# Kernel optimization log

Hardware: AMD Instinct MI355X
Metric: run time of the kernel (lower is better)

The kernel has to match this reference:

```python
import jax, jax.numpy as jnp
import numpy as np

NDIM = 1024
NHEAD = 16
HEAD_DIM = NDIM // NHEAD


def setup_inputs() -> dict:
    key = jax.random.key(0)
    ks = jax.random.split(key, 12)
    B, L, C = 2, 2048, NDIM
    s = 0.02
    return {
        "q": jax.random.normal(ks[0], (B, L, C), jnp.float32),
        "k": jax.random.normal(ks[1], (B, L, C), jnp.float32),
        "v": jax.random.normal(ks[2], (B, L, C), jnp.float32),
        "Wq": jax.random.normal(ks[3], (C, C), jnp.float32) * s,
        "bq": jax.random.normal(ks[4], (C,), jnp.float32) * s,
        "Wk": jax.random.normal(ks[5], (C, C), jnp.float32) * s,
        "bk": jax.random.normal(ks[6], (C,), jnp.float32) * s,
        "Wv": jax.random.normal(ks[7], (C, C), jnp.float32) * s,
        "bv": jax.random.normal(ks[8], (C,), jnp.float32) * s,
        "Wo": jax.random.normal(ks[9], (C, C), jnp.float32) * s,
        "bo": jax.random.normal(ks[10], (C,), jnp.float32) * s,
    }


def reference(q, k, v, Wq, bq, Wk, bk, Wv, bv, Wo, bo):
    B, Lq, C = q.shape
    H, D = NHEAD, HEAD_DIM
    # projections, then split heads: (B, H, L, D)
    qh = (q @ Wq + bq).reshape(B, Lq, H, D).transpose(0, 2, 1, 3)
    kh = (k @ Wk + bk).reshape(B, k.shape[1], H, D).transpose(0, 2, 1, 3)
    vh = (v @ Wv + bv).reshape(B, v.shape[1], H, D).transpose(0, 2, 1, 3)
    scale = 1.0 / jnp.sqrt(jnp.asarray(D, qh.dtype))
    att = jnp.einsum("bhqd,bhkd->bhqk", qh, kh) * scale  # (B,H,Lq,Lk)
    att = jax.nn.softmax(att, axis=-1)  # dropout p=0.0 -> identity
    y = jnp.einsum("bhqk,bhkd->bhqd", att, vh)
    y = y.transpose(0, 2, 1, 3).reshape(B, Lq, C)
    return y @ Wo + bo
```

## Files before the change

### kernel.cpp

```cpp
#include <hip/hip_runtime.h>
#include <math.h>

#define BATCH 2
#define SEQ   2048
#define CDIM  1024
#define NHEAD 16
#define HDIM  64
#define TOKS  (BATCH * SEQ)

typedef __bf16 bf16x8 __attribute__((ext_vector_type(8)));
typedef __bf16 bf16x2 __attribute__((ext_vector_type(2)));
typedef float  f32x4  __attribute__((ext_vector_type(4)));
typedef float  f32x16 __attribute__((ext_vector_type(16)));

#define MFMA16(a, b, c) __builtin_amdgcn_mfma_f32_16x16x32_bf16(a, b, c, 0, 0, 0)
#define MFMA32(a, b, c) __builtin_amdgcn_mfma_f32_32x32x16_bf16(a, b, c, 0, 0, 0)

#define QSCALE 0.1803368801111204f

__device__ __forceinline__ void gload_lds16(const __bf16* g, __bf16* l) {
    __builtin_amdgcn_global_load_lds(
        (const __attribute__((address_space(1))) unsigned int*)g,
        (__attribute__((address_space(3))) unsigned int*)l, 16, 0, 0);
}

__global__ __launch_bounds__(256) void prep_kernel(
    const float* __restrict__ q, const float* __restrict__ k, const float* __restrict__ v,
    __bf16* __restrict__ qo, __bf16* __restrict__ ko, __bf16* __restrict__ vo,
    const float* __restrict__ W0, const float* __restrict__ W1,
    const float* __restrict__ W2, const float* __restrict__ W3,
    __bf16* __restrict__ T0, __bf16* __restrict__ T1,
    __bf16* __restrict__ T2, __bf16* __restrict__ T3)
{
    __shared__ __bf16 Ts[64][72];
    const int bx = blockIdx.x;
    const int tid = threadIdx.x;

    if (bx < 6144) {
        const int t = bx >> 11;
        const size_t i = ((size_t)(bx & 2047) * 256 + tid) * 8;
        const float* s = t == 0 ? q : (t == 1 ? k : v);
        __bf16* d = t == 0 ? qo : (t == 1 ? ko : vo);
        const float4 x = *(const float4*)&s[i];
        const float4 y = *(const float4*)&s[i + 4];
        bf16x8 o;
        o[0] = (__bf16)x.x; o[1] = (__bf16)x.y; o[2] = (__bf16)x.z; o[3] = (__bf16)x.w;
        o[4] = (__bf16)y.x; o[5] = (__bf16)y.y; o[6] = (__bf16)y.z; o[7] = (__bf16)y.w;
        *(bf16x8*)&d[i] = o;
        return;
    }

    const int t  = bx - 6144;
    const int z  = t >> 8;
    const int ry = (t & 255) >> 4;
    const int rx = t & 15;
    const float* W = z == 0 ? W0 : z == 1 ? W1 : z == 2 ? W2 : W3;
    __bf16* T = z == 0 ? T0 : z == 1 ? T1 : z == 2 ? T2 : T3;
    const int rb = ry * 64, cb = rx * 64;
    const int r = tid >> 4;
    const int c4 = (tid & 15) * 4;
#pragma unroll
    for (int p = 0; p < 4; p++) {
        const int rr = p * 16 + r;
        const float4 w4 = *(const float4*)&W[(size_t)(rb + rr) * CDIM + cb + c4];
        Ts[c4 + 0][rr] = (__bf16)w4.x;
        Ts[c4 + 1][rr] = (__bf16)w4.y;
        Ts[c4 + 2][rr] = (__bf16)w4.z;
        Ts[c4 + 3][rr] = (__bf16)w4.w;
    }
    __syncthreads();
    const int n = tid >> 2;
    const int k16 = (tid & 3) * 16;
    *(bf16x8*)&T[(size_t)(cb + n) * CDIM + rb + k16]     = *(const bf16x8*)&Ts[n][k16];
    *(bf16x8*)&T[(size_t)(cb + n) * CDIM + rb + k16 + 8] = *(const bf16x8*)&Ts[n][k16 + 8];
}

__global__ __launch_bounds__(512, 6) void qkv_gemm_kernel(
    const __bf16* __restrict__ qb, const __bf16* __restrict__ kb,
    const __bf16* __restrict__ vb,
    const __bf16* __restrict__ Wqt, const __bf16* __restrict__ Wkt,
    const __bf16* __restrict__ Wvt,
    const float* __restrict__ bq, const float* __restrict__ bk,
    const float* __restrict__ bv,
    __bf16* __restrict__ Qh, __bf16* __restrict__ Kh, __bf16* __restrict__ Vht)
{
    __shared__ __bf16 As[128 * 32];
    __shared__ __bf16 Bs[128 * 32];

    const int lin = blockIdx.x + (blockIdx.y << 3) + (blockIdx.z << 8);
    const int nl  = (lin & 7) * 96 + (lin >> 3);
    const int bx  = nl & 7;
    const int by  = (nl >> 3) & 31;
    const int z   = nl >> 8;

    const __bf16* A    = z == 0 ? qb : z == 1 ? kb : Wvt;
    const __bf16* Bt   = z == 0 ? Wqt : z == 1 ? Wkt : vb;
    const float*  bias = z == 0 ? bq : z == 1 ? bk : bv;

    const int tid  = threadIdx.x;
    const int w    = tid >> 6;
    const int lane = tid & 63;
    const int quad = lane >> 4;
    const int c    = lane & 15;
    const int wm   = w >> 1;
    const int wn   = w & 1;
    const int rowBase = (z == 2 ? bx : by) * 128;
    const int colBase = (z == 2 ? by : bx) * 128;

    const int sr = lane >> 2;
    const int sk = (lane & 3) * 8;

    f32x4 acc[2][4];
#pragma unroll
    for (int i = 0; i < 2; i++)
#pragma unroll
        for (int j = 0; j < 4; j++) acc[i][j] = (f32x4){0, 0, 0, 0};

    const __bf16* srcA = A  + (size_t)(rowBase + w * 16 + sr) * CDIM + sk;
    const __bf16* srcB = Bt + (size_t)(colBase + w * 16 + sr) * CDIM + sk;
    __bf16* dstA = &As[w * 16 * 32];
    __bf16* dstB = &Bs[w * 16 * 32];

    for (int k0 = 0; k0 < CDIM; k0 += 32) {
        gload_lds16(srcA + k0, dstA);
        gload_lds16(srcB + k0, dstB);
        __syncthreads();

        bf16x8 af[2], bf[4];
#pragma unroll
        for (int i = 0; i < 2; i++)
            af[i] = *(const bf16x8*)&As[(wm * 32 + i * 16 + c) * 32 + quad * 8];
#pragma unroll
        for (int i = 0; i < 4; i++)
            bf[i] = *(const bf16x8*)&Bs[(wn * 64 + i * 16 + c) * 32 + quad * 8];
#pragma unroll
        for (int mi = 0; mi < 2; mi++)
#pragma unroll
            for (int ni = 0; ni < 4; ni++)
                acc[mi][ni] = MFMA16(af[mi], bf[ni], acc[mi][ni]);
        __syncthreads();
    }

#pragma unroll
    for (int mi = 0; mi < 2; mi++) {
#pragma unroll
        for (int ni = 0; ni < 4; ni++) {
            const int col = colBase + wn * 64 + ni * 16 + c;
#pragma unroll
            for (int r = 0; r < 4; r++) {
                const int row = rowBase + wm * 32 + mi * 16 + quad * 4 + r;
                const float val = acc[mi][ni][r];
                if (z == 2) {
                    Vht[(size_t)row * TOKS + col] = (__bf16)(val + bias[row]);
                } else {
                    const int b = row >> 11, l = row & 2047;
                    const int h = col >> 6,  d = col & 63;
                    const float s = (z == 0) ? QSCALE : 1.0f;
                    __bf16* outp = (z == 0) ? Qh : Kh;
                    outp[((((size_t)b * NHEAD + h) * SEQ) + l) * HDIM + d] =
                        (__bf16)((val + bias[col]) * s);
                }
            }
        }
    }
}

__global__ __launch_bounds__(512, 4) void out_gemm_kernel(
    const __bf16* __restrict__ A, const __bf16* __restrict__ Bt,
    const float* __restrict__ bias, float* __restrict__ out)
{
    __shared__ __bf16 As[128 * 32];
    __shared__ __bf16 Bs[64 * 32];

    const int lin = blockIdx.x + (blockIdx.y << 4);
    const int nl  = (lin & 7) * 64 + (lin >> 3);
    const int bx  = nl & 15;
    const int by  = nl >> 4;

    const int tid  = threadIdx.x;
    const int w    = tid >> 6;
    const int lane = tid & 63;
    const int quad = lane >> 4;
    const int c    = lane & 15;
    const int wm   = w >> 1;
    const int wn   = w & 1;
    const int rowBase = by * 128;
    const int colBase = bx * 64;
    const int sr = lane >> 2;
    const int sk = (lane & 3) * 8;

    f32x4 acc[2][2];
#pragma unroll
    for (int i = 0; i < 2; i++)
#pragma unroll
        for (int j = 0; j < 2; j++) acc[i][j] = (f32x4){0, 0, 0, 0};

    const __bf16* srcA = A + (size_t)(rowBase + w * 16 + sr) * CDIM + sk;
    const __bf16* srcB = Bt + (size_t)(colBase + (w & 3) * 16 + sr) * CDIM + sk;
    __bf16* dstA = &As[w * 16 * 32];
    __bf16* dstB = &Bs[(w & 3) * 16 * 32];

    for (int k0 = 0; k0 < CDIM; k0 += 32) {
        gload_lds16(srcA + k0, dstA);
        if (w < 4) gload_lds16(srcB + k0, dstB);
        __syncthreads();

        bf16x8 af[2], bf[2];
#pragma unroll
        for (int i = 0; i < 2; i++)
            af[i] = *(const bf16x8*)&As[(wm * 32 + i * 16 + c) * 32 + quad * 8];
#pragma unroll
        for (int i = 0; i < 2; i++)
            bf[i] = *(const bf16x8*)&Bs[(wn * 32 + i * 16 + c) * 32 + quad * 8];
#pragma unroll
        for (int mi = 0; mi < 2; mi++)
#pragma unroll
            for (int ni = 0; ni < 2; ni++)
                acc[mi][ni] = MFMA16(af[mi], bf[ni], acc[mi][ni]);
        __syncthreads();
    }

#pragma unroll
    for (int mi = 0; mi < 2; mi++) {
#pragma unroll
        for (int ni = 0; ni < 2; ni++) {
            const int col = colBase + wn * 32 + ni * 16 + c;
#pragma unroll
            for (int r = 0; r < 4; r++) {
                const int row = rowBase + wm * 32 + mi * 16 + quad * 4 + r;
                out[(size_t)row * CDIM + col] = acc[mi][ni][r] + bias[col];
            }
        }
    }
}

__global__ __launch_bounds__(256, 2) void attn_v8_kernel(
    const __bf16* __restrict__ Qh, const __bf16* __restrict__ Kh,
    const __bf16* __restrict__ Vht, __bf16* __restrict__ Y)
{
    __shared__ __align__(16) __bf16 Ks[2][64][72];
    __shared__ __align__(16) __bf16 Vt[2][64][72];

    const int tid  = threadIdx.x;
    const int w    = tid >> 6;
    const int lane = tid & 63;
    const int l31  = lane & 31;
    const int hi   = lane >> 5;
    const int bh   = blockIdx.x;
    const int b    = bh >> 4;
    const int h    = bh & 15;
    const int qbase = blockIdx.y * 128 + w * 32;

    const __bf16* Qg = Qh + (size_t)bh * SEQ * HDIM;
    const __bf16* Kg = Kh + (size_t)bh * SEQ * HDIM;
    const __bf16* Vg = Vht + (size_t)(h * HDIM) * TOKS + (size_t)b * SEQ;

    bf16x8 qf[4];
#pragma unroll
    for (int ks = 0; ks < 4; ks++)
        qf[ks] = *(const bf16x8*)&Qg[(size_t)(qbase + l31) * HDIM + ks * 16 + hi * 8];

    bf16x8 ones;
#pragma unroll
    for (int j = 0; j < 8; j++) ones[j] = (__bf16)1.0f;

    f32x16 O[2], LA;
#pragma unroll
    for (int j = 0; j < 16; j++) { O[0][j] = 0.0f; O[1][j] = 0.0f; LA[j] = 0.0f; }

    const int srow = tid >> 2;
    const int scol = (tid & 3) * 16;

    *(bf16x8*)&Ks[0][srow][scol]     = *(const bf16x8*)&Kg[(size_t)srow * HDIM + scol];
    *(bf16x8*)&Ks[0][srow][scol + 8] = *(const bf16x8*)&Kg[(size_t)srow * HDIM + scol + 8];
    *(bf16x8*)&Vt[0][srow][scol]     = *(const bf16x8*)&Vg[(size_t)srow * TOKS + scol];
    *(bf16x8*)&Vt[0][srow][scol + 8] = *(const bf16x8*)&Vg[(size_t)srow * TOKS + scol + 8];
    __syncthreads();

    int buf = 0;
    for (int t0 = 0; t0 < SEQ; t0 += 64) {
        const int tn = t0 + 64;
        bf16x8 kp0, kp1, vp0, vp1;
        if (tn < SEQ) {
            kp0 = *(const bf16x8*)&Kg[(size_t)(tn + srow) * HDIM + scol];
            kp1 = *(const bf16x8*)&Kg[(size_t)(tn + srow) * HDIM + scol + 8];
            vp0 = *(const bf16x8*)&Vg[(size_t)srow * TOKS + tn + scol];
            vp1 = *(const bf16x8*)&Vg[(size_t)srow * TOKS + tn + scol + 8];
        }

#pragma unroll
        for (int kt = 0; kt < 2; kt++) {
            f32x16 st0, st1;
#pragma unroll
            for (int j = 0; j < 16; j++) { st0[j] = 0.0f; st1[j] = 0.0f; }
            const bf16x8 kf0 = *(const bf16x8*)&Ks[buf][kt * 32 + l31][hi * 8];
            const bf16x8 kf1 = *(const bf16x8*)&Ks[buf][kt * 32 + l31][16 + hi * 8];
            const bf16x8 kf2 = *(const bf16x8*)&Ks[buf][kt * 32 + l31][32 + hi * 8];
            const bf16x8 kf3 = *(const bf16x8*)&Ks[buf][kt * 32 + l31][48 + hi * 8];
            st0 = MFMA32(kf0, qf[0], st0);
            st1 = MFMA32(kf1, qf[1], st1);
            st0 = MFMA32(kf2, qf[2], st0);
            st1 = MFMA32(kf3, qf[3], st1);

            float p[16];
#pragma unroll
            for (int j = 0; j < 16; j++)
                p[j] = __builtin_amdgcn_exp2f(st0[j] + st1[j]);

#pragma unroll
            for (int kl = 0; kl < 2; kl++) {
                const int r0 = kl * 8;
                union { bf16x2 v; unsigned int u; } pa, pb, pc, pd;
                pa.v[0] = (__bf16)p[r0 + 0]; pa.v[1] = (__bf16)p[r0 + 1];
                pb.v[0] = (__bf16)p[r0 + 2]; pb.v[1] = (__bf16)p[r0 + 3];
                pc.v[0] = (__bf16)p[r0 + 4]; pc.v[1] = (__bf16)p[r0 + 5];
                pd.v[0] = (__bf16)p[r0 + 6]; pd.v[1] = (__bf16)p[r0 + 7];
                asm volatile("v_permlane32_swap_b32 %0, %1"
                             : "+v"(pa.u), "+v"(pc.u));
                asm volatile("v_permlane32_swap_b32 %0, %1"
                             : "+v"(pb.u), "+v"(pd.u));
                union { unsigned int u[4]; bf16x8 v; } af;
                af.u[0] = pa.u; af.u[1] = pb.u; af.u[2] = pc.u; af.u[3] = pd.u;
                const int kcol = kt * 32 + kl * 16 + hi * 8;
                __builtin_amdgcn_s_setprio(1);
                LA = MFMA32(af.v, ones, LA);
#pragma unroll
                for (int dt = 0; dt < 2; dt++) {
                    const bf16x8 vf =
                        *(const bf16x8*)&Vt[buf][dt * 32 + l31][kcol];
                    O[dt] = MFMA32(af.v, vf, O[dt]);
                }
                __builtin_amdgcn_s_setprio(0);
            }
        }

        if (tn < SEQ) {
            *(bf16x8*)&Ks[buf ^ 1][srow][scol]     = kp0;
            *(bf16x8*)&Ks[buf ^ 1][srow][scol + 8] = kp1;
            *(bf16x8*)&Vt[buf ^ 1][srow][scol]     = vp0;
            *(bf16x8*)&Vt[buf ^ 1][srow][scol + 8] = vp1;
        }
        __syncthreads();
        buf ^= 1;
    }

    __bf16* Yb = Y + (size_t)b * SEQ * CDIM;
#pragma unroll
    for (int reg = 0; reg < 16; reg++) {
        const int qrow  = (reg & 3) + 8 * (reg >> 2) + 4 * hi;
        const float iq  = 1.0f / LA[reg];
        __bf16* yp = Yb + (size_t)(qbase + qrow) * CDIM + h * HDIM + l31;
        yp[0]  = (__bf16)(O[0][reg] * iq);
        yp[32] = (__bf16)(O[1][reg] * iq);
    }
}


extern "C" void kernel_launch(void* const* d_in, const int* in_sizes, int n_in,
                              void* d_out, int out_size, void* d_ws, size_t ws_size,
                              hipStream_t stream)
{
    const float* q  = (const float*)d_in[0];
    const float* k  = (const float*)d_in[1];
    const float* v  = (const float*)d_in[2];
    const float* Wq = (const float*)d_in[3];
    const float* bq = (const float*)d_in[4];
    const float* Wk = (const float*)d_in[5];
    const float* bk = (const float*)d_in[6];
    const float* Wv = (const float*)d_in[7];
    const float* bv = (const float*)d_in[8];
    const float* Wo = (const float*)d_in[9];
    const float* bo = (const float*)d_in[10];
    float* out = (float*)d_out;

    const size_t MAT = (size_t)TOKS * CDIM;
    const size_t WN  = (size_t)CDIM * CDIM;

    __bf16* p   = (__bf16*)d_ws;
    __bf16* qb  = p; p += MAT;
    __bf16* kb  = p; p += MAT;
    __bf16* vb  = p; p += MAT;
    __bf16* Wqt = p; p += WN;
    __bf16* Wkt = p; p += WN;
    __bf16* Wvt = p; p += WN;
    __bf16* Wot = p; p += WN;
    __bf16* Qh  = p; p += MAT;
    __bf16* Kh  = p; p += MAT;
    __bf16* Vht = p; p += MAT;
    __bf16* Yb  = qb;

    prep_kernel<<<dim3(7168), dim3(256), 0, stream>>>(
        q, k, v, qb, kb, vb, Wq, Wk, Wv, Wo, Wqt, Wkt, Wvt, Wot);

    qkv_gemm_kernel<<<dim3(8, 32, 3), dim3(512), 0, stream>>>(
        qb, kb, vb, Wqt, Wkt, Wvt, bq, bk, bv, Qh, Kh, Vht);

    attn_v8_kernel<<<dim3(BATCH * NHEAD, SEQ / 128), dim3(256), 0, stream>>>(Qh, Kh, Vht, Yb);

    out_gemm_kernel<<<dim3(16, 32), dim3(512), 0, stream>>>(Yb, Wot, bo, out);
}
```

Baseline: 218.2 us.

## Load K/V fragments directly from global into registers, dropping LDS staging

The attention kernel no longer stages K and V tiles through double-buffered shared memory with block-wide barriers. Each lane now loads its MFMA operand fragments straight from global memory into registers, ping-ponging two K register sets so the next tile's load overlaps the current tile's compute. This removes the LDS writes and reads and the per-tile __syncthreads. In exchange each of the four waves loads the same K/V data separately (4x global/L2 traffic), and register pressure rises, which may hurt occupancy.

```diff
diff --git a/kernel.cpp b/kernel.cpp
--- a/kernel.cpp
+++ b/kernel.cpp
@@ -234,13 +234,71 @@
     }
 }
 
-__global__ __launch_bounds__(256, 2) void attn_v8_kernel(
+__device__ __forceinline__ void attn_load_k(const __bf16* kp, bf16x8 (&K)[8]) {
+#pragma unroll
+    for (int kt = 0; kt < 2; kt++)
+#pragma unroll
+        for (int ks = 0; ks < 4; ks++)
+            K[kt * 4 + ks] = *(const bf16x8*)(kp + (size_t)kt * 32 * HDIM + ks * 16);
+}
+
+__device__ __forceinline__ void attn_load_v(const __bf16* vp, bf16x8 (&V)[8]) {
+#pragma unroll
+    for (int dt = 0; dt < 2; dt++)
+#pragma unroll
+        for (int kt = 0; kt < 2; kt++)
+#pragma unroll
+            for (int kl = 0; kl < 2; kl++)
+                V[dt * 4 + kt * 2 + kl] =
+                    *(const bf16x8*)(vp + (size_t)dt * 32 * TOKS + kt * 32 + kl * 16);
+}
+
+__device__ __forceinline__ void attn_tile(
+    const bf16x8 (&K)[8], const bf16x8 (&V)[8], const bf16x8 (&qf)[4],
+    const bf16x8& ones, f32x16& O0, f32x16& O1, f32x16& LA)
+{
+#pragma unroll
+    for (int kt = 0; kt < 2; kt++) {
+        f32x16 st0, st1;
+#pragma unroll
+        for (int j = 0; j < 16; j++) { st0[j] = 0.0f; st1[j] = 0.0f; }
+        st0 = MFMA32(K[kt * 4 + 0], qf[0], st0);
+        st1 = MFMA32(K[kt * 4 + 1], qf[1], st1);
+        st0 = MFMA32(K[kt * 4 + 2], qf[2], st0);
+        st1 = MFMA32(K[kt * 4 + 3], qf[3], st1);
+
+        float p[16];
+#pragma unroll
+        for (int j = 0; j < 16; j++)
+            p[j] = __builtin_amdgcn_exp2f(st0[j] + st1[j]);
+
+#pragma unroll
+        for (int kl = 0; kl < 2; kl++) {
+            const int r0 = kl * 8;
+            union { bf16x2 v; unsigned int u; } pa, pb, pc, pd;
+            pa.v[0] = (__bf16)p[r0 + 0]; pa.v[1] = (__bf16)p[r0 + 1];
+            pb.v[0] = (__bf16)p[r0 + 2]; pb.v[1] = (__bf16)p[r0 + 3];
+            pc.v[0] = (__bf16)p[r0 + 4]; pc.v[1] = (__bf16)p[r0 + 5];
+            pd.v[0] = (__bf16)p[r0 + 6]; pd.v[1] = (__bf16)p[r0 + 7];
+            asm volatile("v_permlane32_swap_b32 %0, %1"
+                         : "+v"(pa.u), "+v"(pc.u));
+            asm volatile("v_permlane32_swap_b32 %0, %1"
+                         : "+v"(pb.u), "+v"(pd.u));
+            union { unsigned int u[4]; bf16x8 v; } af;
+            af.u[0] = pa.u; af.u[1] = pb.u; af.u[2] = pc.u; af.u[3] = pd.u;
+            __builtin_amdgcn_s_setprio(1);
+            LA = MFMA32(af.v, ones, LA);
+            O0 = MFMA32(af.v, V[0 + kt * 2 + kl], O0);
+            O1 = MFMA32(af.v, V[4 + kt * 2 + kl], O1);
+            __builtin_amdgcn_s_setprio(0);
+        }
+    }
+}
+
+__global__ __launch_bounds__(256, 2) void attn_v9_kernel(
     const __bf16* __restrict__ Qh, const __bf16* __restrict__ Kh,
     const __bf16* __restrict__ Vht, __bf16* __restrict__ Y)
 {
-    __shared__ __align__(16) __bf16 Ks[2][64][72];
-    __shared__ __align__(16) __bf16 Vt[2][64][72];
-
     const int tid  = threadIdx.x;
     const int w    = tid >> 6;
     const int lane = tid & 63;
@@ -264,85 +322,34 @@
 #pragma unroll
     for (int j = 0; j < 8; j++) ones[j] = (__bf16)1.0f;
 
-    f32x16 O[2], LA;
-#pragma unroll
-    for (int j = 0; j < 16; j++) { O[0][j] = 0.0f; O[1][j] = 0.0f; LA[j] = 0.0f; }
-
-    const int srow = tid >> 2;
-    const int scol = (tid & 3) * 16;
-
-    *(bf16x8*)&Ks[0][srow][scol]     = *(const bf16x8*)&Kg[(size_t)srow * HDIM + scol];
-    *(bf16x8*)&Ks[0][srow][scol + 8] = *(const bf16x8*)&Kg[(size_t)srow * HDIM + scol + 8];
-    *(bf16x8*)&Vt[0][srow][scol]     = *(const bf16x8*)&Vg[(size_t)srow * TOKS + scol];
-    *(bf16x8*)&Vt[0][srow][scol + 8] = *(const bf16x8*)&Vg[(size_t)srow * TOKS + scol + 8];
-    __syncthreads();
-
-    int buf = 0;
-    for (int t0 = 0; t0 < SEQ; t0 += 64) {
-        const int tn = t0 + 64;
-        bf16x8 kp0, kp1, vp0, vp1;
-        if (tn < SEQ) {
-            kp0 = *(const bf16x8*)&Kg[(size_t)(tn + srow) * HDIM + scol];
-            kp1 = *(const bf16x8*)&Kg[(size_t)(tn + srow) * HDIM + scol + 8];
-            vp0 = *(const bf16x8*)&Vg[(size_t)srow * TOKS + tn + scol];
-            vp1 = *(const bf16x8*)&Vg[(size_t)srow * TOKS + tn + scol + 8];
-        }
-
-#pragma unroll
-        for (int kt = 0; kt < 2; kt++) {
-            f32x16 st0, st1;
-#pragma unroll
-            for (int j = 0; j < 16; j++) { st0[j] = 0.0f; st1[j] = 0.0f; }
-            const bf16x8 kf0 = *(const bf16x8*)&Ks[buf][kt * 32 + l31][hi * 8];
-            const bf16x8 kf1 = *(const bf16x8*)&Ks[buf][kt * 32 + l31][16 + hi * 8];
-            const bf16x8 kf2 = *(const bf16x8*)&Ks[buf][kt * 32 + l31][32 + hi * 8];
-            const bf16x8 kf3 = *(const bf16x8*)&Ks[buf][kt * 32 + l31][48 + hi * 8];
-            st0 = MFMA32(kf0, qf[0], st0);
-            st1 = MFMA32(kf1, qf[1], st1);
-            st0 = MFMA32(kf2, qf[2], st0);
-            st1 = MFMA32(kf3, qf[3], st1);
-
-            float p[16];
-#pragma unroll
-            for (int j = 0; j < 16; j++)
-                p[j] = __builtin_amdgcn_exp2f(st0[j] + st1[j]);
-
-#pragma unroll
-            for (int kl = 0; kl < 2; kl++) {
-                const int r0 = kl * 8;
-                union { bf16x2 v; unsigned int u; } pa, pb, pc, pd;
-                pa.v[0] = (__bf16)p[r0 + 0]; pa.v[1] = (__bf16)p[r0 + 1];
-                pb.v[0] = (__bf16)p[r0 + 2]; pb.v[1] = (__bf16)p[r0 + 3];
-                pc.v[0] = (__bf16)p[r0 + 4]; pc.v[1] = (__bf16)p[r0 + 5];
-                pd.v[0] = (__bf16)p[r0 + 6]; pd.v[1] = (__bf16)p[r0 + 7];
-                asm volatile("v_permlane32_swap_b32 %0, %1"
-                             : "+v"(pa.u), "+v"(pc.u));
-                asm volatile("v_permlane32_swap_b32 %0, %1"
-                             : "+v"(pb.u), "+v"(pd.u));
-                union { unsigned int u[4]; bf16x8 v; } af;
-                af.u[0] = pa.u; af.u[1] = pb.u; af.u[2] = pc.u; af.u[3] = pd.u;
-                const int kcol = kt * 32 + kl * 16 + hi * 8;
-                __builtin_amdgcn_s_setprio(1);
-                LA = MFMA32(af.v, ones, LA);
-#pragma unroll
-                for (int dt = 0; dt < 2; dt++) {
-                    const bf16x8 vf =
-                        *(const bf16x8*)&Vt[buf][dt * 32 + l31][kcol];
-                    O[dt] = MFMA32(af.v, vf, O[dt]);
-                }
-                __builtin_amdgcn_s_setprio(0);
-            }
-        }
-
-        if (tn < SEQ) {
-            *(bf16x8*)&Ks[buf ^ 1][srow][scol]     = kp0;
-            *(bf16x8*)&Ks[buf ^ 1][srow][scol + 8] = kp1;
-            *(bf16x8*)&Vt[buf ^ 1][srow][scol]     = vp0;
-            *(bf16x8*)&Vt[buf ^ 1][srow][scol + 8] = vp1;
-        }
-        __syncthreads();
-        buf ^= 1;
-    }
+    f32x16 O0, O1, LA;
+#pragma unroll
+    for (int j = 0; j < 16; j++) { O0[j] = 0.0f; O1[j] = 0.0f; LA[j] = 0.0f; }
+
+    const __bf16* kLane = Kg + (size_t)l31 * HDIM + hi * 8;
+    const __bf16* vLane = Vg + (size_t)l31 * TOKS + hi * 8;
+
+    bf16x8 KA[8], KB[8], VV[8];
+    attn_load_k(kLane, KA);
+    const __bf16* kp = kLane + 64 * HDIM;
+    const __bf16* vp = vLane;
+
+    for (int i = 0; i < 15; i++) {
+        attn_load_v(vp, VV);
+        attn_load_k(kp, KB);
+        attn_tile(KA, VV, qf, ones, O0, O1, LA);
+        vp += 64; kp += 64 * HDIM;
+        attn_load_v(vp, VV);
+        attn_load_k(kp, KA);
+        attn_tile(KB, VV, qf, ones, O0, O1, LA);
+        vp += 64; kp += 64 * HDIM;
+    }
+    attn_load_v(vp, VV);
+    attn_load_k(kp, KB);
+    attn_tile(KA, VV, qf, ones, O0, O1, LA);
+    vp += 64;
+    attn_load_v(vp, VV);
+    attn_tile(KB, VV, qf, ones, O0, O1, LA);
 
     __bf16* Yb = Y + (size_t)b * SEQ * CDIM;
 #pragma unroll
@@ -350,8 +357,8 @@
         const int qrow  = (reg & 3) + 8 * (reg >> 2) + 4 * hi;
         const float iq  = 1.0f / LA[reg];
         __bf16* yp = Yb + (size_t)(qbase + qrow) * CDIM + h * HDIM + l31;
-        yp[0]  = (__bf16)(O[0][reg] * iq);
-        yp[32] = (__bf16)(O[1][reg] * iq);
+        yp[0]  = (__bf16)(O0[reg] * iq);
+        yp[32] = (__bf16)(O1[reg] * iq);
     }
 }
 
@@ -395,7 +402,7 @@
     qkv_gemm_kernel<<<dim3(8, 32, 3), dim3(512), 0, stream>>>(
         qb, kb, vb, Wqt, Wkt, Wvt, bq, bk, bv, Qh, Kh, Vht);
 
-    attn_v8_kernel<<<dim3(BATCH * NHEAD, SEQ / 128), dim3(256), 0, stream>>>(Qh, Kh, Vht, Yb);
+    attn_v9_kernel<<<dim3(BATCH * NHEAD, SEQ / 128), dim3(256), 0, stream>>>(Qh, Kh, Vht, Yb);
 
     out_gemm_kernel<<<dim3(16, 32), dim3(512), 0, stream>>>(Yb, Wot, bo, out);
 }
```

Result: slower. 286.7 us (+31.4%).

## Stage attention K/V tiles via direct global-to-LDS loads with XOR swizzle

Applied to the files above, without the earlier changes.

The attention kernel now stages K and V tiles with global_load_lds (direct to LDS, no register round-trip), doubles the key tile from 64 to 128 tokens per iteration, and replaces LDS row padding with an XOR swizzle to avoid bank conflicts. This removes the VGPR staging and explicit LDS stores and halves the barrier count. In exchange it doubles LDS use per block (64KB), which may limit occupancy. The async loads also rely on the loop-end barrier for correctness.

```diff
diff --git a/kernel.cpp b/kernel.cpp
--- a/kernel.cpp
+++ b/kernel.cpp
@@ -234,18 +234,19 @@
     }
 }
 
-__global__ __launch_bounds__(256, 2) void attn_v8_kernel(
+__global__ __launch_bounds__(256, 2) void attn_v10_kernel(
     const __bf16* __restrict__ Qh, const __bf16* __restrict__ Kh,
     const __bf16* __restrict__ Vht, __bf16* __restrict__ Y)
 {
-    __shared__ __align__(16) __bf16 Ks[2][64][72];
-    __shared__ __align__(16) __bf16 Vt[2][64][72];
+    __shared__ __align__(16) __bf16 Ks[2][128][64];
+    __shared__ __align__(16) __bf16 Vt[2][64][128];
 
     const int tid  = threadIdx.x;
     const int w    = tid >> 6;
     const int lane = tid & 63;
     const int l31  = lane & 31;
     const int hi   = lane >> 5;
+    const int swz  = l31 & 7;
     const int bh   = blockIdx.x;
     const int b    = bh >> 4;
     const int h    = bh & 15;
@@ -264,39 +265,46 @@
 #pragma unroll
     for (int j = 0; j < 8; j++) ones[j] = (__bf16)1.0f;
 
-    f32x16 O[2], LA;
-#pragma unroll
-    for (int j = 0; j < 16; j++) { O[0][j] = 0.0f; O[1][j] = 0.0f; LA[j] = 0.0f; }
-
-    const int srow = tid >> 2;
-    const int scol = (tid & 3) * 16;
-
-    *(bf16x8*)&Ks[0][srow][scol]     = *(const bf16x8*)&Kg[(size_t)srow * HDIM + scol];
-    *(bf16x8*)&Ks[0][srow][scol + 8] = *(const bf16x8*)&Kg[(size_t)srow * HDIM + scol + 8];
-    *(bf16x8*)&Vt[0][srow][scol]     = *(const bf16x8*)&Vg[(size_t)srow * TOKS + scol];
-    *(bf16x8*)&Vt[0][srow][scol + 8] = *(const bf16x8*)&Vg[(size_t)srow * TOKS + scol + 8];
+    f32x16 O0, O1, LA;
+#pragma unroll
+    for (int j = 0; j < 16; j++) { O0[j] = 0.0f; O1[j] = 0.0f; LA[j] = 0.0f; }
+
+    const int kr8 = lane >> 3, kc = lane & 7;
+    const int vr4 = lane >> 4, vc = lane & 15;
+
+#define STAGE(T, bb)                                                          \
+    {                                                                         \
+        _Pragma("unroll")                                                     \
+        for (int jj = 0; jj < 4; jj++) {                                      \
+            const int j = w * 4 + jj;                                         \
+            gload_lds16(Kg + (size_t)((T) + 8 * j + kr8) * HDIM               \
+                           + ((kc ^ kr8) * 8),                                \
+                        &Ks[bb][8 * j][0]);                                   \
+            gload_lds16(Vg + (size_t)(4 * j + vr4) * TOKS + (T)               \
+                           + ((vc ^ ((4 * j + vr4) & 7)) * 8),                \
+                        &Vt[bb][4 * j][0]);                                   \
+        }                                                                     \
+    }
+
+    STAGE(0, 0);
     __syncthreads();
 
     int buf = 0;
-    for (int t0 = 0; t0 < SEQ; t0 += 64) {
-        const int tn = t0 + 64;
-        bf16x8 kp0, kp1, vp0, vp1;
+    for (int t0 = 0; t0 < SEQ; t0 += 128) {
+        const int tn = t0 + 128;
         if (tn < SEQ) {
-            kp0 = *(const bf16x8*)&Kg[(size_t)(tn + srow) * HDIM + scol];
-            kp1 = *(const bf16x8*)&Kg[(size_t)(tn + srow) * HDIM + scol + 8];
-            vp0 = *(const bf16x8*)&Vg[(size_t)srow * TOKS + tn + scol];
-            vp1 = *(const bf16x8*)&Vg[(size_t)srow * TOKS + tn + scol + 8];
+            if (buf == 0) STAGE(tn, 1) else STAGE(tn, 0)
         }
 
 #pragma unroll
-        for (int kt = 0; kt < 2; kt++) {
+        for (int kt = 0; kt < 4; kt++) {
             f32x16 st0, st1;
 #pragma unroll
             for (int j = 0; j < 16; j++) { st0[j] = 0.0f; st1[j] = 0.0f; }
-            const bf16x8 kf0 = *(const bf16x8*)&Ks[buf][kt * 32 + l31][hi * 8];
-            const bf16x8 kf1 = *(const bf16x8*)&Ks[buf][kt * 32 + l31][16 + hi * 8];
-            const bf16x8 kf2 = *(const bf16x8*)&Ks[buf][kt * 32 + l31][32 + hi * 8];
-            const bf16x8 kf3 = *(const bf16x8*)&Ks[buf][kt * 32 + l31][48 + hi * 8];
+            const bf16x8 kf0 = *(const bf16x8*)&Ks[buf][kt * 32 + l31][((0 + hi) ^ swz) * 8];
+            const bf16x8 kf1 = *(const bf16x8*)&Ks[buf][kt * 32 + l31][((2 + hi) ^ swz) * 8];
+            const bf16x8 kf2 = *(const bf16x8*)&Ks[buf][kt * 32 + l31][((4 + hi) ^ swz) * 8];
+            const bf16x8 kf3 = *(const bf16x8*)&Ks[buf][kt * 32 + l31][((6 + hi) ^ swz) * 8];
             st0 = MFMA32(kf0, qf[0], st0);
             st1 = MFMA32(kf1, qf[1], st1);
             st0 = MFMA32(kf2, qf[2], st0);
@@ -321,28 +329,21 @@
                              : "+v"(pb.u), "+v"(pd.u));
                 union { unsigned int u[4]; bf16x8 v; } af;
                 af.u[0] = pa.u; af.u[1] = pb.u; af.u[2] = pc.u; af.u[3] = pd.u;
-                const int kcol = kt * 32 + kl * 16 + hi * 8;
+                const int cc = kt * 4 + kl * 2 + hi;
+                const bf16x8 vf0 = *(const bf16x8*)&Vt[buf][l31][(cc ^ swz) * 8];
+                const bf16x8 vf1 = *(const bf16x8*)&Vt[buf][32 + l31][(cc ^ swz) * 8];
                 __builtin_amdgcn_s_setprio(1);
                 LA = MFMA32(af.v, ones, LA);
-#pragma unroll
-                for (int dt = 0; dt < 2; dt++) {
-                    const bf16x8 vf =
-                        *(const bf16x8*)&Vt[buf][dt * 32 + l31][kcol];
-                    O[dt] = MFMA32(af.v, vf, O[dt]);
-                }
+                O0 = MFMA32(af.v, vf0, O0);
+                O1 = MFMA32(af.v, vf1, O1);
                 __builtin_amdgcn_s_setprio(0);
             }
         }
 
-        if (tn < SEQ) {
-            *(bf16x8*)&Ks[buf ^ 1][srow][scol]     = kp0;
-            *(bf16x8*)&Ks[buf ^ 1][srow][scol + 8] = kp1;
-            *(bf16x8*)&Vt[buf ^ 1][srow][scol]     = vp0;
-            *(bf16x8*)&Vt[buf ^ 1][srow][scol + 8] = vp1;
-        }
         __syncthreads();
         buf ^= 1;
     }
+#undef STAGE
 
     __bf16* Yb = Y + (size_t)b * SEQ * CDIM;
 #pragma unroll
@@ -350,8 +351,8 @@
         const int qrow  = (reg & 3) + 8 * (reg >> 2) + 4 * hi;
         const float iq  = 1.0f / LA[reg];
         __bf16* yp = Yb + (size_t)(qbase + qrow) * CDIM + h * HDIM + l31;
-        yp[0]  = (__bf16)(O[0][reg] * iq);
-        yp[32] = (__bf16)(O[1][reg] * iq);
+        yp[0]  = (__bf16)(O0[reg] * iq);
+        yp[32] = (__bf16)(O1[reg] * iq);
     }
 }
 
@@ -395,7 +396,7 @@
     qkv_gemm_kernel<<<dim3(8, 32, 3), dim3(512), 0, stream>>>(
         qb, kb, vb, Wqt, Wkt, Wvt, bq, bk, bv, Qh, Kh, Vht);
 
-    attn_v8_kernel<<<dim3(BATCH * NHEAD, SEQ / 128), dim3(256), 0, stream>>>(Qh, Kh, Vht, Yb);
+    attn_v10_kernel<<<dim3(BATCH * NHEAD, SEQ / 128), dim3(256), 0, stream>>>(Qh, Kh, Vht, Yb);
 
     out_gemm_kernel<<<dim3(16, 32), dim3(512), 0, stream>>>(Yb, Wot, bo, out);
 }
```

After: 218.7 us. Within noise of the previous version (+0.2%).
